# Kernel optimization log

Measured on AMD Instinct MI355X. Metric: run time of the kernel, lower is better.

## Reference

```python
import jax, jax.numpy as jnp
import numpy as np
from jax import lax

NUM_BLOCKS = 3
NUM_LAYERS = 10
NL = NUM_BLOCKS * NUM_LAYERS  # 30 res blocks
RC = 512   # residual channels
GC = 512   # gate channels
SC = 512   # skip channels
KS = 2     # kernel size
CIN = 128  # local-conditioning channels
FRONT = 32 # front conv kernel size
OUT = 2    # gaussian (mean, log_std)
UPS = [16, 16]  # upsample scales, product = 256 hop
SQRT_HALF = 0.7071067811865476


def causal_conv1d(x, w, b, dilation):
    # x: [B,C_in,T], w: [C_out,C_in,K] -> left-pad only == torch pad-both + trim right (causal SAME)
    pad = dilation * (w.shape[-1] - 1)
    y = lax.conv_general_dilated(x, w, window_strides=(1,), padding=[(pad, 0)],
                                 rhs_dilation=(dilation,),
                                 dimension_numbers=('NCH', 'OIH', 'NCH'))
    return y + b[None, :, None]


def pw(x, w, b):
    # 1x1 conv: w [C_out,C_in]
    return jnp.einsum('oi,bit->bot', w, x) + b[None, :, None]


def upsample(c, up_w, up_b):
    # c: [B,CIN,Tm]; torch ConvTranspose2d(1,1,(3,2s),pad=(1,s//2),stride=(1,s)) + LeakyReLU(0.4)
    h = c[:, None]  # [B,1,CIN,Tm]
    for j, s in enumerate(UPS):
        k = up_w[j][:, :, ::-1, ::-1]  # flip kernel: transposed conv as lhs-dilated conv
        pw_ = 2 * s - 1 - s // 2       # = K - 1 - torch_pad along width
        h = lax.conv_general_dilated(h, k, window_strides=(1, 1),
                                     padding=[(1, 1), (pw_, pw_)],
                                     lhs_dilation=(1, s),
                                     dimension_numbers=('NCHW', 'OIHW', 'NCHW')) + up_b[j]
        h = jnp.where(h > 0, h, 0.4 * h)  # LeakyReLU(0.4)
    return h[:, 0]  # [B,CIN,T]


def setup_inputs() -> dict:
    key = jax.random.key(0)
    ks = iter(jax.random.split(key, 32))
    def rn(shape, scale):
        return jax.random.normal(next(ks), shape, dtype=jnp.float32) * scale
    B, T_mel = 1, 16
    T = T_mel * 256
    return {
        'x': rn((B, 1, T), 1.0),
        'c': rn((B, CIN, T_mel), 1.0),
        'front_w': rn((RC, 1, FRONT), 0.2),
        'front_b': rn((RC,), 0.05),
        'filt_w': rn((NL, GC, RC, KS), 0.03),
        'filt_b': rn((NL, GC), 0.05),
        'gate_w': rn((NL, GC, RC, KS), 0.03),
        'gate_b': rn((NL, GC), 0.05),
        'cf_w': rn((NL, GC, CIN), 0.05),
        'cf_b': rn((NL, GC), 0.05),
        'cg_w': rn((NL, GC, CIN), 0.05),
        'cg_b': rn((NL, GC), 0.05),
        'res_w': rn((NL, RC, GC), 0.04),
        'res_b': rn((NL, RC), 0.05),
        'skip_w': rn((NL, SC, GC), 0.04),
        'skip_b': rn((NL, SC), 0.05),
        'fin1_w': rn((SC, SC), 0.04),
        'fin1_b': rn((SC,), 0.05),
        'fin2_w': rn((OUT, SC), 0.04),
        'fin2_b': rn((OUT,), 0.05),
        'up_w': rn((2, 1, 1, 3, 2 * 16), 0.1),
        'up_b': rn((2,), 0.05),
    }


def reference(x, c, front_w, front_b, filt_w, filt_b, gate_w, gate_b,
              cf_w, cf_b, cg_w, cg_b, res_w, res_b, skip_w, skip_b,
              fin1_w, fin1_b, fin2_w, fin2_b, up_w, up_b):
    c_up = upsample(c, up_w, up_b)                       # [B,CIN,T]
    h = jax.nn.relu(causal_conv1d(x, front_w, front_b, 1))  # [B,RC,T]
    skip = jnp.zeros((x.shape[0], SC, x.shape[2]), x.dtype)
    for i in range(NL):
        d = KS ** (i % NUM_LAYERS)
        f = causal_conv1d(h, filt_w[i], filt_b[i], d) + pw(c_up, cf_w[i], cf_b[i])
        g = causal_conv1d(h, gate_w[i], gate_b[i], d) + pw(c_up, cg_w[i], cg_b[i])
        o = jnp.tanh(f) * jax.nn.sigmoid(g)
        h = (h + pw(o, res_w[i], res_b[i])) * SQRT_HALF
        skip = skip + pw(o, skip_w[i], skip_b[i])
    out = jax.nn.relu(skip)
    out = jax.nn.relu(pw(out, fin1_w, fin1_b))
    return pw(out, fin2_w, fin2_b)  # [B,OUT,T]
```

## Files before the change

kernel.cpp:

```cpp
#include <hip/hip_runtime.h>
#include <hip/hip_bf16.h>

#define TLEN 4096
#define HPADT 512
#define SQRT_HALF 0.70710678118654752f

typedef __attribute__((ext_vector_type(8))) short short8;
typedef __attribute__((ext_vector_type(4))) float floatx4;
typedef __attribute__((ext_vector_type(4))) unsigned short ushort4v;

#define MFMA_BF16(a, b, c) __builtin_amdgcn_mfma_f32_16x16x32_bf16((a), (b), (c), 0, 0, 0)

__device__ __forceinline__ float bf2f(unsigned short u) {
  union { unsigned int i; float f; } v; v.i = ((unsigned int)u) << 16; return v.f;
}
__device__ __forceinline__ unsigned short f2bf(float x) {
  union { float f; unsigned int i; } v; v.f = x;
  unsigned int r = v.i + 0x7FFFu + ((v.i >> 16) & 1u);
  return (unsigned short)(r >> 16);
}
__device__ __forceinline__ short8 ld8(const unsigned short* p) { return *(const short8*)p; }

template <int NI>
__device__ __forceinline__ void stage128(unsigned short* lds, const unsigned short* src,
                                         int stride, int tid) {
  #pragma unroll
  for (int inst = 0; inst < NI; ++inst) {
    int qb = inst * 256 + (tid & 192);
    int q = qb + (tid & 63);
    int r = q >> 4;
    int c = (q & 15) ^ (r & 15);
    __builtin_amdgcn_global_load_lds(
        (const __attribute__((address_space(1))) unsigned int*)(src + (size_t)r * stride + (c << 3)),
        (__attribute__((address_space(3))) unsigned int*)(lds + qb * 8),
        16, 0, 0);
  }
}

__device__ __forceinline__ short8 frag128(const unsigned short* lds, int r, int cj) {
  return *(const short8*)(lds + r * 128 + ((cj ^ (r & 15)) << 3));
}

__global__ __launch_bounds__(256) void cast_all_kernel(
    const float* __restrict__ fw, const float* __restrict__ gw,
    const float* __restrict__ rw, const float* __restrict__ sw,
    const float* __restrict__ cf, const float* __restrict__ cg,
    const float* __restrict__ f1, const float* __restrict__ fb,
    const float* __restrict__ cfb, const float* __restrict__ gb,
    const float* __restrict__ cgb,
    unsigned short* __restrict__ WA, unsigned short* __restrict__ RS,
    unsigned short* __restrict__ CA, unsigned short* __restrict__ F1c,
    float* __restrict__ fgb)
{
  int b = blockIdx.x;
  if (b < 7680) {
    size_t idx = (size_t)b * 256 + threadIdx.x;
    size_t l = idx >> 16;
    int o = (int)((idx >> 7) & 511);
    int i4 = (int)(idx & 127) * 4;
    const float4* fp = (const float4*)(fw + (((l * 512 + o) * 512 + i4) * 2));
    const float4* gp = (const float4*)(gw + (((l * 512 + o) * 512 + i4) * 2));
    float4 f0 = fp[0], f1v = fp[1];
    float4 g0 = gp[0], g1 = gp[1];
    size_t base0 = ((l * 2 + 0) * 1024);
    size_t base1 = ((l * 2 + 1) * 1024);
    *(ushort4v*)&WA[(base0 + o) * 512 + i4]       = (ushort4v){f2bf(f0.x), f2bf(f0.z), f2bf(f1v.x), f2bf(f1v.z)};
    *(ushort4v*)&WA[(base1 + o) * 512 + i4]       = (ushort4v){f2bf(f0.y), f2bf(f0.w), f2bf(f1v.y), f2bf(f1v.w)};
    *(ushort4v*)&WA[(base0 + 512 + o) * 512 + i4] = (ushort4v){f2bf(g0.x), f2bf(g0.z), f2bf(g1.x), f2bf(g1.z)};
    *(ushort4v*)&WA[(base1 + 512 + o) * 512 + i4] = (ushort4v){f2bf(g0.y), f2bf(g0.w), f2bf(g1.y), f2bf(g1.w)};
  } else if (b < 15360) {
    size_t idx = (size_t)(b - 7680) * 256 + threadIdx.x;
    size_t l = idx >> 16;
    int o = (int)((idx >> 7) & 511);
    int i4 = (int)(idx & 127) * 4;
    float4 r4 = *(const float4*)(rw + ((l * 512 + o) * 512 + i4));
    float4 s4 = *(const float4*)(sw + ((l * 512 + o) * 512 + i4));
    *(ushort4v*)&RS[(l * 1024 + o) * 512 + i4]       = (ushort4v){f2bf(r4.x), f2bf(r4.y), f2bf(r4.z), f2bf(r4.w)};
    *(ushort4v*)&RS[(l * 1024 + 512 + o) * 512 + i4] = (ushort4v){f2bf(s4.x), f2bf(s4.y), f2bf(s4.z), f2bf(s4.w)};
  } else if (b < 17280) {
    size_t idx = (size_t)(b - 15360) * 256 + threadIdx.x;
    size_t l = idx >> 14;
    int o = (int)((idx >> 5) & 511);
    int i4 = (int)(idx & 31) * 4;
    float4 f4 = *(const float4*)(cf + ((l * 512 + o) * 128 + i4));
    float4 g4 = *(const float4*)(cg + ((l * 512 + o) * 128 + i4));
    *(ushort4v*)&CA[(l * 1024 + o) * 128 + i4]       = (ushort4v){f2bf(f4.x), f2bf(f4.y), f2bf(f4.z), f2bf(f4.w)};
    *(ushort4v*)&CA[(l * 1024 + 512 + o) * 128 + i4] = (ushort4v){f2bf(g4.x), f2bf(g4.y), f2bf(g4.z), f2bf(g4.w)};
  } else if (b < 17536) {
    size_t idx = (size_t)(b - 17280) * 256 + threadIdx.x;
    float4 v = *(const float4*)(f1 + idx * 4);
    *(ushort4v*)&F1c[idx * 4] = (ushort4v){f2bf(v.x), f2bf(v.y), f2bf(v.z), f2bf(v.w)};
  } else {
    int idx = (b - 17536) * 256 + threadIdx.x;
    int l = idx >> 10, r = idx & 1023;
    float v;
    if (r < 512) v = fb[l * 512 + r] + cfb[l * 512 + r];
    else         v = gb[l * 512 + r - 512] + cgb[l * 512 + r - 512];
    fgb[idx] = v;
  }
}


__global__ __launch_bounds__(256) void upsample1_kernel(
    const float* __restrict__ c, const float* __restrict__ up_w,
    const float* __restrict__ up_b, float* __restrict__ u1)
{
  int x = threadIdx.x;
  int h = blockIdx.x;
  const float* w = up_w;
  float acc = 0.f;
  int k1 = (23 - x) & 15;
  #pragma unroll
  for (int dk = 0; dk < 2; ++dk) {
    int kx = k1 + 16 * dk;
    int num = x + kx - 23;
    if (num >= 0) {
      int qq = num >> 4;
      if (qq < 16) {
        #pragma unroll
        for (int ky = 0; ky < 3; ++ky) {
          int hh = h + ky - 1;
          if (hh >= 0 && hh < 128)
            acc += c[hh * 16 + qq] * w[(2 - ky) * 32 + (31 - kx)];
        }
      }
    }
  }
  acc += up_b[0];
  u1[h * 256 + x] = acc > 0.f ? acc : 0.4f * acc;
}

__global__ __launch_bounds__(256) void upsample2_kernel(
    const float* __restrict__ u1, const float* __restrict__ up_w,
    const float* __restrict__ up_b, unsigned short* __restrict__ cu)
{
  int x = blockIdx.x * 256 + threadIdx.x;
  int h = blockIdx.y;
  const float* w = up_w + 96;
  float acc = 0.f;
  int k1 = (23 - x) & 15;
  #pragma unroll
  for (int dk = 0; dk < 2; ++dk) {
    int kx = k1 + 16 * dk;
    int num = x + kx - 23;
    if (num >= 0) {
      int qq = num >> 4;
      if (qq < 256) {
        #pragma unroll
        for (int ky = 0; ky < 3; ++ky) {
          int hh = h + ky - 1;
          if (hh >= 0 && hh < 128)
            acc += u1[hh * 256 + qq] * w[(2 - ky) * 32 + (31 - kx)];
        }
      }
    }
  }
  acc += up_b[1];
  acc = acc > 0.f ? acc : 0.4f * acc;
  cu[(size_t)x * 128 + h] = f2bf(acc);
}

__global__ __launch_bounds__(256) void front_kernel(
    const float* __restrict__ x, const float* __restrict__ fw, const float* __restrict__ fb,
    float* __restrict__ hf, unsigned short* __restrict__ hbf)
{
  __shared__ float xs[40];
  int tid = threadIdx.x;
  int o = blockIdx.y * 256 + tid;
  int t0 = blockIdx.x * 8;
  if (tid < 39) {
    int gx = t0 - 31 + tid;
    xs[tid] = (gx >= 0) ? x[gx] : 0.f;
  }
  __syncthreads();
  float w[32];
  #pragma unroll
  for (int k = 0; k < 32; ++k) w[k] = fw[o * 32 + k];
  float b = fb[o];
  #pragma unroll
  for (int j = 0; j < 8; ++j) {
    float acc = b;
    #pragma unroll
    for (int k = 0; k < 32; ++k) acc += w[k] * xs[j + k];
    acc = acc > 0.f ? acc : 0.f;
    int t = t0 + j;
    hf[(size_t)t * 512 + o] = acc;
    hbf[(size_t)(HPADT + t) * 512 + o] = f2bf(acc);
  }
}

__global__ __launch_bounds__(256) void gemm_a_kernel(
    const unsigned short* __restrict__ WA,
    const unsigned short* __restrict__ CA,
    const float* __restrict__ fgb,
    const unsigned short* __restrict__ hbf,
    const unsigned short* __restrict__ cu,
    unsigned short* __restrict__ obf,
    const int d)
{
  __shared__ unsigned short Af[2][64 * 128];
  __shared__ unsigned short Ag[2][64 * 128];
  __shared__ unsigned short Xs[2][128 * 128];

  const int tid = threadIdx.x;
  const int lane = tid & 63;
  const int wave = tid >> 6;
  const int lm = lane & 15, qd = lane >> 4;
  const int n0 = blockIdx.x * 128;
  const int m0 = blockIdx.y * 64;
  const int wm = (wave & 1) * 32;
  const int wn = (wave >> 1) * 64;

  floatx4 accF[2][4], accG[2][4];
  #pragma unroll
  for (int a = 0; a < 2; ++a)
    #pragma unroll
    for (int b = 0; b < 4; ++b) {
      accF[a][b] = (floatx4){0.f, 0.f, 0.f, 0.f};
      accG[a][b] = (floatx4){0.f, 0.f, 0.f, 0.f};
    }

  auto stage_step = [&](int s, int b) {
    if (s < 8) {
      int tap = s >> 2;
      int k0 = (s & 3) * 128;
      const unsigned short* ab = WA + (size_t)tap * 524288;
      stage128<4>(&Af[b][0], ab + (size_t)m0 * 512 + k0, 512, tid);
      stage128<4>(&Ag[b][0], ab + (size_t)(512 + m0) * 512 + k0, 512, tid);
      stage128<8>(&Xs[b][0], hbf + (size_t)(HPADT + n0 - (tap ? 0 : d)) * 512 + k0, 512, tid);
    } else {
      stage128<4>(&Af[b][0], CA + (size_t)m0 * 128, 128, tid);
      stage128<4>(&Ag[b][0], CA + (size_t)(512 + m0) * 128, 128, tid);
      stage128<8>(&Xs[b][0], cu + (size_t)n0 * 128, 128, tid);
    }
  };

  stage_step(0, 0);
  for (int s = 0; s < 9; ++s) {
    __syncthreads();
    if (s < 8) stage_step(s + 1, (s + 1) & 1);
    const unsigned short* af = &Af[s & 1][0];
    const unsigned short* ag = &Ag[s & 1][0];
    const unsigned short* xs = &Xs[s & 1][0];
    #pragma unroll
    for (int j = 0; j < 4; ++j) {
      int cj = j * 4 + qd;
      short8 a[2], g[2], xv[4];
      a[0] = frag128(af, wm + lm, cj);
      a[1] = frag128(af, wm + 16 + lm, cj);
      g[0] = frag128(ag, wm + lm, cj);
      g[1] = frag128(ag, wm + 16 + lm, cj);
      #pragma unroll
      for (int nt = 0; nt < 4; ++nt) xv[nt] = frag128(xs, wn + nt * 16 + lm, cj);
      #pragma unroll
      for (int mt = 0; mt < 2; ++mt)
        #pragma unroll
        for (int nt = 0; nt < 4; ++nt) {
          accF[mt][nt] = MFMA_BF16(a[mt], xv[nt], accF[mt][nt]);
          accG[mt][nt] = MFMA_BF16(g[mt], xv[nt], accG[mt][nt]);
        }
    }
  }

  #pragma unroll
  for (int mt = 0; mt < 2; ++mt) {
    int oc0 = m0 + wm + mt * 16 + qd * 4;
    floatx4 fb4 = *(const floatx4*)&fgb[oc0];
    floatx4 gb4 = *(const floatx4*)&fgb[512 + oc0];
    #pragma unroll
    for (int nt = 0; nt < 4; ++nt) {
      int t = n0 + wn + nt * 16 + lm;
      ushort4v o4;
      #pragma unroll
      for (int r = 0; r < 4; ++r) {
        float f = accF[mt][nt][r] + fb4[r];
        float g = accG[mt][nt][r] + gb4[r];
        float ef = __expf(-2.f * f);
        float th = (1.f - ef) / (1.f + ef);
        float sg = 1.f / (1.f + __expf(-g));
        o4[r] = f2bf(th * sg);
      }
      *(ushort4v*)&obf[(size_t)t * 512 + oc0] = o4;
    }
  }
}

__global__ __launch_bounds__(256) void gemm_b_kernel(
    const unsigned short* __restrict__ RS,
    const float* __restrict__ rb, const float* __restrict__ sb,
    const unsigned short* __restrict__ obf,
    float* __restrict__ hf, unsigned short* __restrict__ hbf,
    float* __restrict__ skip, unsigned short* __restrict__ skipbf,
    const int first, const int last)
{
  __shared__ unsigned short Ar[2][64 * 128];
  __shared__ unsigned short As_[2][64 * 128];
  __shared__ unsigned short Xs[2][128 * 128];

  const int tid = threadIdx.x;
  const int lane = tid & 63;
  const int wave = tid >> 6;
  const int lm = lane & 15, qd = lane >> 4;
  const int n0 = blockIdx.x * 128;
  const int m0 = blockIdx.y * 64;
  const int wm = (wave & 1) * 32;
  const int wn = (wave >> 1) * 64;

  floatx4 accR[2][4], accS[2][4];
  #pragma unroll
  for (int a = 0; a < 2; ++a)
    #pragma unroll
    for (int b = 0; b < 4; ++b) {
      accR[a][b] = (floatx4){0.f, 0.f, 0.f, 0.f};
      accS[a][b] = (floatx4){0.f, 0.f, 0.f, 0.f};
    }

  auto stage_step = [&](int s, int b) {
    int k0 = s * 128;
    stage128<4>(&Ar[b][0], RS + (size_t)m0 * 512 + k0, 512, tid);
    stage128<4>(&As_[b][0], RS + (size_t)(512 + m0) * 512 + k0, 512, tid);
    stage128<8>(&Xs[b][0], obf + (size_t)n0 * 512 + k0, 512, tid);
  };

  stage_step(0, 0);
  for (int s = 0; s < 4; ++s) {
    __syncthreads();
    if (s < 3) stage_step(s + 1, (s + 1) & 1);
    const unsigned short* ar = &Ar[s & 1][0];
    const unsigned short* as = &As_[s & 1][0];
    const unsigned short* xs = &Xs[s & 1][0];
    #pragma unroll
    for (int j = 0; j < 4; ++j) {
      int cj = j * 4 + qd;
      short8 a[2], g[2], xv[4];
      a[0] = frag128(ar, wm + lm, cj);
      a[1] = frag128(ar, wm + 16 + lm, cj);
      g[0] = frag128(as, wm + lm, cj);
      g[1] = frag128(as, wm + 16 + lm, cj);
      #pragma unroll
      for (int nt = 0; nt < 4; ++nt) xv[nt] = frag128(xs, wn + nt * 16 + lm, cj);
      #pragma unroll
      for (int mt = 0; mt < 2; ++mt)
        #pragma unroll
        for (int nt = 0; nt < 4; ++nt) {
          accR[mt][nt] = MFMA_BF16(a[mt], xv[nt], accR[mt][nt]);
          accS[mt][nt] = MFMA_BF16(g[mt], xv[nt], accS[mt][nt]);
        }
    }
  }

  #pragma unroll
  for (int mt = 0; mt < 2; ++mt) {
    int oc0 = m0 + wm + mt * 16 + qd * 4;
    floatx4 rb4 = *(const floatx4*)&rb[oc0];
    floatx4 sb4 = *(const floatx4*)&sb[oc0];
    #pragma unroll
    for (int nt = 0; nt < 4; ++nt) {
      int t = n0 + wn + nt * 16 + lm;
      size_t base = (size_t)t * 512 + oc0;
      floatx4 h4 = *(const floatx4*)&hf[base];
      floatx4 s4;
      if (first) s4 = (floatx4){0.f, 0.f, 0.f, 0.f};
      else s4 = *(const floatx4*)&skip[base];
      ushort4v hb4;
      #pragma unroll
      for (int r = 0; r < 4; ++r) {
        float hv = (h4[r] + accR[mt][nt][r] + rb4[r]) * SQRT_HALF;
        h4[r] = hv;
        hb4[r] = f2bf(hv);
        s4[r] = s4[r] + accS[mt][nt][r] + sb4[r];
      }
      *(floatx4*)&hf[base] = h4;
      *(ushort4v*)&hbf[(size_t)(HPADT + t) * 512 + oc0] = hb4;
      *(floatx4*)&skip[base] = s4;
      if (last) {
        ushort4v sk4;
        #pragma unroll
        for (int r = 0; r < 4; ++r) sk4[r] = f2bf(s4[r] > 0.f ? s4[r] : 0.f);
        *(ushort4v*)&skipbf[base] = sk4;
      }
    }
  }
}

__global__ __launch_bounds__(256) void final1_kernel(
    const unsigned short* __restrict__ W1,
    const float* __restrict__ b1,
    const unsigned short* __restrict__ skipbf,
    unsigned short* __restrict__ t1)
{
  __shared__ unsigned short Aw[2][64 * 128];
  __shared__ unsigned short Xs[2][128 * 128];

  const int tid = threadIdx.x;
  const int lane = tid & 63;
  const int wave = tid >> 6;
  const int lm = lane & 15, qd = lane >> 4;
  const int n0 = blockIdx.x * 128;
  const int m0 = blockIdx.y * 64;
  const int wm = (wave & 1) * 32;
  const int wn = (wave >> 1) * 64;

  floatx4 acc[2][4];
  #pragma unroll
  for (int a = 0; a < 2; ++a)
    #pragma unroll
    for (int b = 0; b < 4; ++b) acc[a][b] = (floatx4){0.f, 0.f, 0.f, 0.f};

  auto stage_step = [&](int s, int b) {
    int k0 = s * 128;
    stage128<4>(&Aw[b][0], W1 + (size_t)m0 * 512 + k0, 512, tid);
    stage128<8>(&Xs[b][0], skipbf + (size_t)n0 * 512 + k0, 512, tid);
  };

  stage_step(0, 0);
  for (int s = 0; s < 4; ++s) {
    __syncthreads();
    if (s < 3) stage_step(s + 1, (s + 1) & 1);
    const unsigned short* aw = &Aw[s & 1][0];
    const unsigned short* xs = &Xs[s & 1][0];
    #pragma unroll
    for (int j = 0; j < 4; ++j) {
      int cj = j * 4 + qd;
      short8 a[2], xv[4];
      a[0] = frag128(aw, wm + lm, cj);
      a[1] = frag128(aw, wm + 16 + lm, cj);
      #pragma unroll
      for (int nt = 0; nt < 4; ++nt) xv[nt] = frag128(xs, wn + nt * 16 + lm, cj);
      #pragma unroll
      for (int mt = 0; mt < 2; ++mt)
        #pragma unroll
        for (int nt = 0; nt < 4; ++nt)
          acc[mt][nt] = MFMA_BF16(a[mt], xv[nt], acc[mt][nt]);
    }
  }

  #pragma unroll
  for (int mt = 0; mt < 2; ++mt) {
    int oc0 = m0 + wm + mt * 16 + qd * 4;
    floatx4 b4 = *(const floatx4*)&b1[oc0];
    #pragma unroll
    for (int nt = 0; nt < 4; ++nt) {
      int t = n0 + wn + nt * 16 + lm;
      ushort4v o4;
      #pragma unroll
      for (int r = 0; r < 4; ++r) {
        float v = acc[mt][nt][r] + b4[r];
        o4[r] = f2bf(v > 0.f ? v : 0.f);
      }
      *(ushort4v*)&t1[(size_t)t * 512 + oc0] = o4;
    }
  }
}

__global__ __launch_bounds__(256) void final2_kernel(
    const float* __restrict__ W2, const float* __restrict__ b2,
    const unsigned short* __restrict__ t1, float* __restrict__ out)
{
  int wave = threadIdx.x >> 6, lane = threadIdx.x & 63;
  int t = blockIdx.x * 4 + wave;
  short8 v = ld8(t1 + (size_t)t * 512 + lane * 8);
  float a0 = 0.f, a1 = 0.f;
  #pragma unroll
  for (int r = 0; r < 8; ++r) {
    float f = bf2f((unsigned short)v[r]);
    a0 += W2[lane * 8 + r] * f;
    a1 += W2[512 + lane * 8 + r] * f;
  }
  #pragma unroll
  for (int off = 32; off > 0; off >>= 1) {
    a0 += __shfl_xor(a0, off, 64);
    a1 += __shfl_xor(a1, off, 64);
  }
  if (lane == 0) {
    out[t] = a0 + b2[0];
    out[TLEN + t] = a1 + b2[1];
  }
}

extern "C" void kernel_launch(void* const* d_in, const int* in_sizes, int n_in,
                              void* d_out, int out_size, void* d_ws, size_t ws_size,
                              hipStream_t stream) {
  (void)in_sizes; (void)n_in; (void)out_size; (void)ws_size;
  const float* x       = (const float*)d_in[0];
  const float* c       = (const float*)d_in[1];
  const float* front_w = (const float*)d_in[2];
  const float* front_b = (const float*)d_in[3];
  const float* filt_w  = (const float*)d_in[4];
  const float* filt_b  = (const float*)d_in[5];
  const float* gate_w  = (const float*)d_in[6];
  const float* gate_b  = (const float*)d_in[7];
  const float* cf_w    = (const float*)d_in[8];
  const float* cf_b    = (const float*)d_in[9];
  const float* cg_w    = (const float*)d_in[10];
  const float* cg_b    = (const float*)d_in[11];
  const float* res_w   = (const float*)d_in[12];
  const float* res_b   = (const float*)d_in[13];
  const float* skip_w  = (const float*)d_in[14];
  const float* skip_b  = (const float*)d_in[15];
  const float* fin1_w  = (const float*)d_in[16];
  const float* fin1_b  = (const float*)d_in[17];
  const float* fin2_w  = (const float*)d_in[18];
  const float* fin2_b  = (const float*)d_in[19];
  const float* up_w    = (const float*)d_in[20];
  const float* up_b    = (const float*)d_in[21];

  char* ws = (char*)d_ws;
  auto alloc = [&](size_t bytes) {
    char* p = ws;
    ws += (bytes + 255) & ~(size_t)255;
    return p;
  };
  unsigned short* WA     = (unsigned short*)alloc((size_t)30 * 2 * 1024 * 512 * 2);
  unsigned short* RS     = (unsigned short*)alloc((size_t)30 * 1024 * 512 * 2);
  unsigned short* CA     = (unsigned short*)alloc((size_t)30 * 1024 * 128 * 2);
  unsigned short* F1c    = (unsigned short*)alloc((size_t)512 * 512 * 2);
  float* fgb             = (float*)alloc((size_t)30 * 1024 * 4);
  float* u1              = (float*)alloc((size_t)128 * 256 * 4);
  unsigned short* cu     = (unsigned short*)alloc((size_t)TLEN * 128 * 2);
  float* hf              = (float*)alloc((size_t)TLEN * 512 * 4);
  unsigned short* hbf    = (unsigned short*)alloc((size_t)(HPADT + TLEN) * 512 * 2);
  unsigned short* obf    = (unsigned short*)alloc((size_t)TLEN * 512 * 2);
  float* skip            = (float*)alloc((size_t)TLEN * 512 * 4);
  unsigned short* skipbf = (unsigned short*)alloc((size_t)TLEN * 512 * 2);
  unsigned short* t1     = (unsigned short*)alloc((size_t)TLEN * 512 * 2);
  float* out             = (float*)d_out;

  hipMemsetAsync(hbf, 0, (size_t)HPADT * 512 * 2, stream);

  cast_all_kernel<<<17656, 256, 0, stream>>>(
      filt_w, gate_w, res_w, skip_w, cf_w, cg_w, fin1_w,
      filt_b, cf_b, gate_b, cg_b, WA, RS, CA, F1c, fgb);

  upsample1_kernel<<<dim3(128), 256, 0, stream>>>(c, up_w, up_b, u1);
  upsample2_kernel<<<dim3(16, 128), 256, 0, stream>>>(u1, up_w, up_b, cu);
  front_kernel<<<dim3(512, 2), 256, 0, stream>>>(x, front_w, front_b, hf, hbf);

  for (int l = 0; l < 30; ++l) {
    int d = 1 << (l % 10);
    gemm_a_kernel<<<dim3(32, 8), 256, 0, stream>>>(
        WA + (size_t)l * 2 * 524288, CA + (size_t)l * 131072,
        fgb + (size_t)l * 1024,
        hbf, cu, obf, d);
    gemm_b_kernel<<<dim3(32, 8), 256, 0, stream>>>(
        RS + (size_t)l * 524288,
        res_b + (size_t)l * 512, skip_b + (size_t)l * 512,
        obf, hf, hbf, skip, skipbf, (l == 0) ? 1 : 0, (l == 29) ? 1 : 0);
  }

  final1_kernel<<<dim3(32, 8), 256, 0, stream>>>(F1c, fin1_b, skipbf, t1);
  final2_kernel<<<1024, 256, 0, stream>>>(fin2_w, fin2_b, t1, out);
}
```

Measured before the change: 1.287 ms.

## Fuse all residual layers into one persistent kernel with grid barriers

Replaces the 60 per-layer GEMM launches with a single persistent kernel of 256 blocks that loops over all 30 layers and uses atomic grid barriers between the gate GEMM and the residual/skip GEMM. The residual state h and the skip accumulator stay in registers across layers, so the fp32 hf/skip global reads and writes are removed. The first residual-weight tile is also prefetched while the gate stage finishes. The cost is 60 spin-wait grid barriers, and the design relies on all 256 blocks being resident at once, which a normal launch does not guarantee.

```diff
diff --git a/kernel.cpp b/kernel.cpp
--- a/kernel.cpp
+++ b/kernel.cpp
@@ -39,6 +39,18 @@
 
 __device__ __forceinline__ short8 frag128(const unsigned short* lds, int r, int cj) {
   return *(const short8*)(lds + r * 128 + ((cj ^ (r & 15)) << 3));
+}
+
+__device__ __forceinline__ void grid_barrier(int* bar, int target) {
+  __threadfence();
+  __syncthreads();
+  if (threadIdx.x == 0) {
+    atomicAdd(bar, 1);
+    while (__hip_atomic_load(bar, __ATOMIC_RELAXED, __HIP_MEMORY_SCOPE_AGENT) < target)
+      __builtin_amdgcn_s_sleep(2);
+  }
+  __syncthreads();
+  __threadfence();
 }
 
 __global__ __launch_bounds__(256) void cast_all_kernel(
@@ -189,14 +201,19 @@
   }
 }
 
-__global__ __launch_bounds__(256) void gemm_a_kernel(
-    const unsigned short* __restrict__ WA,
-    const unsigned short* __restrict__ CA,
-    const float* __restrict__ fgb,
-    const unsigned short* __restrict__ hbf,
+__global__ __launch_bounds__(256, 1) void wavenet_main_kernel(
+    const unsigned short* __restrict__ WA_all,
+    const unsigned short* __restrict__ RS_all,
+    const unsigned short* __restrict__ CA_all,
+    const float* __restrict__ fgb_all,
+    const float* __restrict__ rb_all,
+    const float* __restrict__ sb_all,
     const unsigned short* __restrict__ cu,
+    const float* __restrict__ hf_init,
+    unsigned short* __restrict__ hbf,
     unsigned short* __restrict__ obf,
-    const int d)
+    unsigned short* __restrict__ skipbf,
+    int* __restrict__ bar)
 {
   __shared__ unsigned short Af[2][64 * 128];
   __shared__ unsigned short Ag[2][64 * 128];
@@ -206,179 +223,199 @@
   const int lane = tid & 63;
   const int wave = tid >> 6;
   const int lm = lane & 15, qd = lane >> 4;
-  const int n0 = blockIdx.x * 128;
-  const int m0 = blockIdx.y * 64;
+  const int n0 = (blockIdx.x & 31) * 128;
+  const int m0 = (blockIdx.x >> 5) * 64;
   const int wm = (wave & 1) * 32;
   const int wn = (wave >> 1) * 64;
 
-  floatx4 accF[2][4], accG[2][4];
-  #pragma unroll
-  for (int a = 0; a < 2; ++a)
-    #pragma unroll
-    for (int b = 0; b < 4; ++b) {
-      accF[a][b] = (floatx4){0.f, 0.f, 0.f, 0.f};
-      accG[a][b] = (floatx4){0.f, 0.f, 0.f, 0.f};
-    }
-
-  auto stage_step = [&](int s, int b) {
-    if (s < 8) {
-      int tap = s >> 2;
-      int k0 = (s & 3) * 128;
-      const unsigned short* ab = WA + (size_t)tap * 524288;
-      stage128<4>(&Af[b][0], ab + (size_t)m0 * 512 + k0, 512, tid);
-      stage128<4>(&Ag[b][0], ab + (size_t)(512 + m0) * 512 + k0, 512, tid);
-      stage128<8>(&Xs[b][0], hbf + (size_t)(HPADT + n0 - (tap ? 0 : d)) * 512 + k0, 512, tid);
-    } else {
-      stage128<4>(&Af[b][0], CA + (size_t)m0 * 128, 128, tid);
-      stage128<4>(&Ag[b][0], CA + (size_t)(512 + m0) * 128, 128, tid);
-      stage128<8>(&Xs[b][0], cu + (size_t)n0 * 128, 128, tid);
-    }
-  };
-
-  stage_step(0, 0);
-  for (int s = 0; s < 9; ++s) {
-    __syncthreads();
-    if (s < 8) stage_step(s + 1, (s + 1) & 1);
-    const unsigned short* af = &Af[s & 1][0];
-    const unsigned short* ag = &Ag[s & 1][0];
-    const unsigned short* xs = &Xs[s & 1][0];
-    #pragma unroll
-    for (int j = 0; j < 4; ++j) {
-      int cj = j * 4 + qd;
-      short8 a[2], g[2], xv[4];
-      a[0] = frag128(af, wm + lm, cj);
-      a[1] = frag128(af, wm + 16 + lm, cj);
-      g[0] = frag128(ag, wm + lm, cj);
-      g[1] = frag128(ag, wm + 16 + lm, cj);
-      #pragma unroll
-      for (int nt = 0; nt < 4; ++nt) xv[nt] = frag128(xs, wn + nt * 16 + lm, cj);
-      #pragma unroll
-      for (int mt = 0; mt < 2; ++mt)
-        #pragma unroll
-        for (int nt = 0; nt < 4; ++nt) {
-          accF[mt][nt] = MFMA_BF16(a[mt], xv[nt], accF[mt][nt]);
-          accG[mt][nt] = MFMA_BF16(g[mt], xv[nt], accG[mt][nt]);
-        }
-    }
-  }
-
+  floatx4 hfr[2][4], skr[2][4];
   #pragma unroll
   for (int mt = 0; mt < 2; ++mt) {
     int oc0 = m0 + wm + mt * 16 + qd * 4;
-    floatx4 fb4 = *(const floatx4*)&fgb[oc0];
-    floatx4 gb4 = *(const floatx4*)&fgb[512 + oc0];
     #pragma unroll
     for (int nt = 0; nt < 4; ++nt) {
       int t = n0 + wn + nt * 16 + lm;
-      ushort4v o4;
-      #pragma unroll
-      for (int r = 0; r < 4; ++r) {
-        float f = accF[mt][nt][r] + fb4[r];
-        float g = accG[mt][nt][r] + gb4[r];
-        float ef = __expf(-2.f * f);
-        float th = (1.f - ef) / (1.f + ef);
-        float sg = 1.f / (1.f + __expf(-g));
-        o4[r] = f2bf(th * sg);
-      }
-      *(ushort4v*)&obf[(size_t)t * 512 + oc0] = o4;
-    }
-  }
-}
-
-__global__ __launch_bounds__(256) void gemm_b_kernel(
-    const unsigned short* __restrict__ RS,
-    const float* __restrict__ rb, const float* __restrict__ sb,
-    const unsigned short* __restrict__ obf,
-    float* __restrict__ hf, unsigned short* __restrict__ hbf,
-    float* __restrict__ skip, unsigned short* __restrict__ skipbf,
-    const int first, const int last)
-{
-  __shared__ unsigned short Ar[2][64 * 128];
-  __shared__ unsigned short As_[2][64 * 128];
-  __shared__ unsigned short Xs[2][128 * 128];
-
-  const int tid = threadIdx.x;
-  const int lane = tid & 63;
-  const int wave = tid >> 6;
-  const int lm = lane & 15, qd = lane >> 4;
-  const int n0 = blockIdx.x * 128;
-  const int m0 = blockIdx.y * 64;
-  const int wm = (wave & 1) * 32;
-  const int wn = (wave >> 1) * 64;
-
-  floatx4 accR[2][4], accS[2][4];
-  #pragma unroll
-  for (int a = 0; a < 2; ++a)
-    #pragma unroll
-    for (int b = 0; b < 4; ++b) {
-      accR[a][b] = (floatx4){0.f, 0.f, 0.f, 0.f};
-      accS[a][b] = (floatx4){0.f, 0.f, 0.f, 0.f};
-    }
-
-  auto stage_step = [&](int s, int b) {
-    int k0 = s * 128;
-    stage128<4>(&Ar[b][0], RS + (size_t)m0 * 512 + k0, 512, tid);
-    stage128<4>(&As_[b][0], RS + (size_t)(512 + m0) * 512 + k0, 512, tid);
-    stage128<8>(&Xs[b][0], obf + (size_t)n0 * 512 + k0, 512, tid);
-  };
-
-  stage_step(0, 0);
-  for (int s = 0; s < 4; ++s) {
-    __syncthreads();
-    if (s < 3) stage_step(s + 1, (s + 1) & 1);
-    const unsigned short* ar = &Ar[s & 1][0];
-    const unsigned short* as = &As_[s & 1][0];
-    const unsigned short* xs = &Xs[s & 1][0];
-    #pragma unroll
-    for (int j = 0; j < 4; ++j) {
-      int cj = j * 4 + qd;
-      short8 a[2], g[2], xv[4];
-      a[0] = frag128(ar, wm + lm, cj);
-      a[1] = frag128(ar, wm + 16 + lm, cj);
-      g[0] = frag128(as, wm + lm, cj);
-      g[1] = frag128(as, wm + 16 + lm, cj);
-      #pragma unroll
-      for (int nt = 0; nt < 4; ++nt) xv[nt] = frag128(xs, wn + nt * 16 + lm, cj);
-      #pragma unroll
-      for (int mt = 0; mt < 2; ++mt)
-        #pragma unroll
-        for (int nt = 0; nt < 4; ++nt) {
-          accR[mt][nt] = MFMA_BF16(a[mt], xv[nt], accR[mt][nt]);
-          accS[mt][nt] = MFMA_BF16(g[mt], xv[nt], accS[mt][nt]);
+      hfr[mt][nt] = *(const floatx4*)&hf_init[(size_t)t * 512 + oc0];
+      skr[mt][nt] = (floatx4){0.f, 0.f, 0.f, 0.f};
+    }
+  }
+
+  int bar_t = 0;
+
+  #pragma unroll 1
+  for (int l = 0; l < 30; ++l) {
+    const int d = 1 << (l % 10);
+    const unsigned short* WA = WA_all + (size_t)l * 2 * 524288;
+    const unsigned short* CA = CA_all + (size_t)l * 131072;
+    const unsigned short* RS = RS_all + (size_t)l * 524288;
+    const float* fgbl = fgb_all + l * 1024;
+    const float* rbl = rb_all + l * 512;
+    const float* sbl = sb_all + l * 512;
+
+    auto stageA_W = [&](int s, int b) {
+      if (s < 8) {
+        int tap = s >> 2, k0 = (s & 3) * 128;
+        const unsigned short* ab = WA + (size_t)tap * 524288;
+        stage128<4>(&Af[b][0], ab + (size_t)m0 * 512 + k0, 512, tid);
+        stage128<4>(&Ag[b][0], ab + (size_t)(512 + m0) * 512 + k0, 512, tid);
+      } else {
+        stage128<4>(&Af[b][0], CA + (size_t)m0 * 128, 128, tid);
+        stage128<4>(&Ag[b][0], CA + (size_t)(512 + m0) * 128, 128, tid);
+      }
+    };
+    auto stageA_X = [&](int s, int b) {
+      if (s < 8) {
+        int tap = s >> 2, k0 = (s & 3) * 128;
+        stage128<8>(&Xs[b][0], hbf + (size_t)(HPADT + n0 - (tap ? 0 : d)) * 512 + k0, 512, tid);
+      } else {
+        stage128<8>(&Xs[b][0], cu + (size_t)n0 * 128, 128, tid);
+      }
+    };
+    auto stageB_W = [&](int s, int b) {
+      int k0 = s * 128;
+      stage128<4>(&Af[b][0], RS + (size_t)m0 * 512 + k0, 512, tid);
+      stage128<4>(&Ag[b][0], RS + (size_t)(512 + m0) * 512 + k0, 512, tid);
+    };
+    auto stageB_X = [&](int s, int b) {
+      stage128<8>(&Xs[b][0], obf + (size_t)n0 * 512 + s * 128, 512, tid);
+    };
+
+    floatx4 accF[2][4], accG[2][4];
+    #pragma unroll
+    for (int a = 0; a < 2; ++a)
+      #pragma unroll
+      for (int b = 0; b < 4; ++b) {
+        accF[a][b] = (floatx4){0.f, 0.f, 0.f, 0.f};
+        accG[a][b] = (floatx4){0.f, 0.f, 0.f, 0.f};
+      }
+
+    stageA_W(0, 0); stageA_X(0, 0);
+    for (int s = 0; s < 9; ++s) {
+      __syncthreads();
+      if (s < 8) { stageA_W(s + 1, (s + 1) & 1); stageA_X(s + 1, (s + 1) & 1); }
+      else       { stageB_W(0, 1); }
+      const unsigned short* af = &Af[s & 1][0];
+      const unsigned short* ag = &Ag[s & 1][0];
+      const unsigned short* xs = &Xs[s & 1][0];
+      #pragma unroll
+      for (int j = 0; j < 4; ++j) {
+        int cj = j * 4 + qd;
+        short8 a[2], g[2], xv[4];
+        a[0] = frag128(af, wm + lm, cj);
+        a[1] = frag128(af, wm + 16 + lm, cj);
+        g[0] = frag128(ag, wm + lm, cj);
+        g[1] = frag128(ag, wm + 16 + lm, cj);
+        #pragma unroll
+        for (int nt = 0; nt < 4; ++nt) xv[nt] = frag128(xs, wn + nt * 16 + lm, cj);
+        #pragma unroll
+        for (int mt = 0; mt < 2; ++mt)
+          #pragma unroll
+          for (int nt = 0; nt < 4; ++nt) {
+            accF[mt][nt] = MFMA_BF16(a[mt], xv[nt], accF[mt][nt]);
+            accG[mt][nt] = MFMA_BF16(g[mt], xv[nt], accG[mt][nt]);
+          }
+      }
+    }
+
+    #pragma unroll
+    for (int mt = 0; mt < 2; ++mt) {
+      int oc0 = m0 + wm + mt * 16 + qd * 4;
+      floatx4 fb4 = *(const floatx4*)&fgbl[oc0];
+      floatx4 gb4 = *(const floatx4*)&fgbl[512 + oc0];
+      #pragma unroll
+      for (int nt = 0; nt < 4; ++nt) {
+        int t = n0 + wn + nt * 16 + lm;
+        ushort4v o4;
+        #pragma unroll
+        for (int r = 0; r < 4; ++r) {
+          float f = accF[mt][nt][r] + fb4[r];
+          float g = accG[mt][nt][r] + gb4[r];
+          float ef = __expf(-2.f * f);
+          float th = (1.f - ef) / (1.f + ef);
+          float sg = 1.f / (1.f + __expf(-g));
+          o4[r] = f2bf(th * sg);
         }
-    }
+        *(ushort4v*)&obf[(size_t)t * 512 + oc0] = o4;
+      }
+    }
+
+    bar_t += 256;
+    grid_barrier(bar, bar_t);
+
+    floatx4 accR[2][4], accS[2][4];
+    #pragma unroll
+    for (int a = 0; a < 2; ++a)
+      #pragma unroll
+      for (int b = 0; b < 4; ++b) {
+        accR[a][b] = (floatx4){0.f, 0.f, 0.f, 0.f};
+        accS[a][b] = (floatx4){0.f, 0.f, 0.f, 0.f};
+      }
+
+    stageB_X(0, 1);
+    for (int s = 0; s < 4; ++s) {
+      __syncthreads();
+      if (s < 3) { int nb = ((s + 1) & 1) ^ 1; stageB_W(s + 1, nb); stageB_X(s + 1, nb); }
+      const int cb = (s & 1) ^ 1;
+      const unsigned short* ar = &Af[cb][0];
+      const unsigned short* as = &Ag[cb][0];
+      const unsigned short* xs = &Xs[cb][0];
+      #pragma unroll
+      for (int j = 0; j < 4; ++j) {
+        int cj = j * 4 + qd;
+        short8 a[2], g[2], xv[4];
+        a[0] = frag128(ar, wm + lm, cj);
+        a[1] = frag128(ar, wm + 16 + lm, cj);
+        g[0] = frag128(as, wm + lm, cj);
+        g[1] = frag128(as, wm + 16 + lm, cj);
+        #pragma unroll
+        for (int nt = 0; nt < 4; ++nt) xv[nt] = frag128(xs, wn + nt * 16 + lm, cj);
+        #pragma unroll
+        for (int mt = 0; mt < 2; ++mt)
+          #pragma unroll
+          for (int nt = 0; nt < 4; ++nt) {
+            accR[mt][nt] = MFMA_BF16(a[mt], xv[nt], accR[mt][nt]);
+            accS[mt][nt] = MFMA_BF16(g[mt], xv[nt], accS[mt][nt]);
+          }
+      }
+    }
+
+    #pragma unroll
+    for (int mt = 0; mt < 2; ++mt) {
+      int oc0 = m0 + wm + mt * 16 + qd * 4;
+      floatx4 rb4 = *(const floatx4*)&rbl[oc0];
+      floatx4 sb4 = *(const floatx4*)&sbl[oc0];
+      #pragma unroll
+      for (int nt = 0; nt < 4; ++nt) {
+        int t = n0 + wn + nt * 16 + lm;
+        ushort4v hb4;
+        #pragma unroll
+        for (int r = 0; r < 4; ++r) {
+          float hv = (hfr[mt][nt][r] + accR[mt][nt][r] + rb4[r]) * SQRT_HALF;
+          hfr[mt][nt][r] = hv;
+          hb4[r] = f2bf(hv);
+          skr[mt][nt][r] += accS[mt][nt][r] + sb4[r];
+        }
+        *(ushort4v*)&hbf[(size_t)(HPADT + t) * 512 + oc0] = hb4;
+      }
+    }
+
+    bar_t += 256;
+    grid_barrier(bar, bar_t);
   }
 
   #pragma unroll
   for (int mt = 0; mt < 2; ++mt) {
     int oc0 = m0 + wm + mt * 16 + qd * 4;
-    floatx4 rb4 = *(const floatx4*)&rb[oc0];
-    floatx4 sb4 = *(const floatx4*)&sb[oc0];
     #pragma unroll
     for (int nt = 0; nt < 4; ++nt) {
       int t = n0 + wn + nt * 16 + lm;
-      size_t base = (size_t)t * 512 + oc0;
-      floatx4 h4 = *(const floatx4*)&hf[base];
-      floatx4 s4;
-      if (first) s4 = (floatx4){0.f, 0.f, 0.f, 0.f};
-      else s4 = *(const floatx4*)&skip[base];
-      ushort4v hb4;
+      ushort4v sk4;
       #pragma unroll
       for (int r = 0; r < 4; ++r) {
-        float hv = (h4[r] + accR[mt][nt][r] + rb4[r]) * SQRT_HALF;
-        h4[r] = hv;
-        hb4[r] = f2bf(hv);
-        s4[r] = s4[r] + accS[mt][nt][r] + sb4[r];
-      }
-      *(floatx4*)&hf[base] = h4;
-      *(ushort4v*)&hbf[(size_t)(HPADT + t) * 512 + oc0] = hb4;
-      *(floatx4*)&skip[base] = s4;
-      if (last) {
-        ushort4v sk4;
-        #pragma unroll
-        for (int r = 0; r < 4; ++r) sk4[r] = f2bf(s4[r] > 0.f ? s4[r] : 0.f);
-        *(ushort4v*)&skipbf[base] = sk4;
-      }
+        float v = skr[mt][nt][r];
+        sk4[r] = f2bf(v > 0.f ? v : 0.f);
+      }
+      *(ushort4v*)&skipbf[(size_t)t * 512 + oc0] = sk4;
     }
   }
 }
@@ -521,12 +558,13 @@
   float* hf              = (float*)alloc((size_t)TLEN * 512 * 4);
   unsigned short* hbf    = (unsigned short*)alloc((size_t)(HPADT + TLEN) * 512 * 2);
   unsigned short* obf    = (unsigned short*)alloc((size_t)TLEN * 512 * 2);
-  float* skip            = (float*)alloc((size_t)TLEN * 512 * 4);
   unsigned short* skipbf = (unsigned short*)alloc((size_t)TLEN * 512 * 2);
   unsigned short* t1     = (unsigned short*)alloc((size_t)TLEN * 512 * 2);
+  int* bar               = (int*)alloc(256);
   float* out             = (float*)d_out;
 
   hipMemsetAsync(hbf, 0, (size_t)HPADT * 512 * 2, stream);
+  hipMemsetAsync(bar, 0, 256, stream);
 
   cast_all_kernel<<<17656, 256, 0, stream>>>(
       filt_w, gate_w, res_w, skip_w, cf_w, cg_w, fin1_w,
@@ -536,17 +574,8 @@
   upsample2_kernel<<<dim3(16, 128), 256, 0, stream>>>(u1, up_w, up_b, cu);
   front_kernel<<<dim3(512, 2), 256, 0, stream>>>(x, front_w, front_b, hf, hbf);
 
-  for (int l = 0; l < 30; ++l) {
-    int d = 1 << (l % 10);
-    gemm_a_kernel<<<dim3(32, 8), 256, 0, stream>>>(
-        WA + (size_t)l * 2 * 524288, CA + (size_t)l * 131072,
-        fgb + (size_t)l * 1024,
-        hbf, cu, obf, d);
-    gemm_b_kernel<<<dim3(32, 8), 256, 0, stream>>>(
-        RS + (size_t)l * 524288,
-        res_b + (size_t)l * 512, skip_b + (size_t)l * 512,
-        obf, hf, hbf, skip, skipbf, (l == 0) ? 1 : 0, (l == 29) ? 1 : 0);
-  }
+  wavenet_main_kernel<<<256, 256, 0, stream>>>(
+      WA, RS, CA, fgb, res_b, skip_b, cu, hf, hbf, obf, skipbf, bar);
 
   final1_kernel<<<dim3(32, 8), 256, 0, stream>>>(F1c, fin1_b, skipbf, t1);
   final2_kernel<<<1024, 256, 0, stream>>>(fin2_w, fin2_b, t1, out);
```

Result: slower. 4.062 ms (+215.5%).
